# Kernel optimization log

Measured on AMD Instinct MI355X. Metric: run time of the kernel, lower is better.

## Reference

```python
import jax, jax.numpy as jnp
import numpy as np

N_NODES = 100000
N_EDGES = 400000
N_REL = 3
N_LAYERS = 2
D = 128          # input feature dim == hidden_dim so weights stack cleanly
N_CLASSES = 2


def setup_inputs() -> dict:
    key = jax.random.key(0)
    ks = jax.random.split(key, 7)
    x = jax.random.normal(ks[0], (N_NODES, D), dtype=jnp.float32)
    edge_index = jax.random.randint(ks[1], (N_REL, 2, N_EDGES), 0, N_NODES, dtype=jnp.int32)
    # SAGEConv params per (layer, relation): neighbor weight, root weight, bias
    Wn = jax.random.normal(ks[2], (N_LAYERS, N_REL, D, D), dtype=jnp.float32) * (1.0 / np.sqrt(D))
    Wr = jax.random.normal(ks[3], (N_LAYERS, N_REL, D, D), dtype=jnp.float32) * (1.0 / np.sqrt(D))
    b = jax.random.normal(ks[4], (N_LAYERS, N_REL, D), dtype=jnp.float32) * 0.02
    Wc = jax.random.normal(ks[5], (D, N_CLASSES), dtype=jnp.float32) * (1.0 / np.sqrt(D))
    bc = jax.random.normal(ks[6], (N_CLASSES,), dtype=jnp.float32) * 0.02
    return {"x": x, "edge_index": edge_index, "Wn": Wn, "Wr": Wr, "b": b, "Wc": Wc, "bc": bc}


def _mean_agg(h, ei, n_nodes):
    # gather source features, scatter-mean into destination nodes
    src, dst = ei[0], ei[1]
    s = jax.ops.segment_sum(h[src], dst, num_segments=n_nodes)          # [N, D]
    cnt = jax.ops.segment_sum(jnp.ones((ei.shape[1],), h.dtype), dst, num_segments=n_nodes)
    return s / jnp.maximum(cnt, 1.0)[:, None]


def reference(x, edge_index, Wn, Wr, b, Wc, bc):
    n = x.shape[0]
    h = x
    L, R = Wn.shape[0], Wn.shape[1]
    for l in range(L):
        out = jnp.zeros((n, Wn.shape[-1]), h.dtype)
        for r in range(R):
            # SAGEConv: lin_l(mean neighbors) + lin_r(root) + bias; HeteroConv sums relations
            agg = _mean_agg(h, edge_index[r], n)
            out = out + agg @ Wn[l, r] + h @ Wr[l, r] + b[l, r]
        h = jax.nn.relu(out) if l < L - 1 else out  # dropout is eval-mode identity
    return h @ Wc + bc
```

## Files before the change

kernel.cpp:

```cpp
#include <hip/hip_runtime.h>

#define NN 100000
#define NE 400000
#define NR 3
#define DD 128
#define NROWS (NR * NN)
#define NEDGES (NR * NE)
#define SCAN_BLOCKS ((NROWS + 1023) / 1024)

typedef float f32x4 __attribute__((ext_vector_type(4)));
typedef __bf16 bf16x8 __attribute__((ext_vector_type(8)));

__device__ __forceinline__ unsigned short f2bf(float f) {
    unsigned int u = __float_as_uint(f);
    u += 0x7fff + ((u >> 16) & 1);
    return (unsigned short)(u >> 16);
}
__device__ __forceinline__ float bflo(unsigned int u) { return __uint_as_float(u << 16); }
__device__ __forceinline__ float bfhi(unsigned int u) { return __uint_as_float(u & 0xffff0000u); }

__device__ __forceinline__ void gload16(const void* g, void* l) {
    __builtin_amdgcn_global_load_lds(
        (const __attribute__((address_space(1))) void*)g,
        (__attribute__((address_space(3))) void*)l, 16, 0, 0);
}

#define NB_CVT 6250
#define NB_WT 512
#define NB_ZERO 586
__global__ __launch_bounds__(256) void prep_all(const float* __restrict__ x,
                                                const float* __restrict__ Wn,
                                                const float* __restrict__ Wr,
                                                const float* __restrict__ b,
                                                unsigned short* __restrict__ xb,
                                                unsigned short* __restrict__ Wt2,
                                                float* __restrict__ bias,
                                                unsigned int* __restrict__ zbase) {
    int bid = blockIdx.x;
    int tid = threadIdx.x;
    if (bid < NB_CVT) {
        int i = bid * 256 + tid;
        const float4* xf = reinterpret_cast<const float4*>(x + (size_t)i * 8);
        float4 a = xf[0], bv = xf[1];
        uint4 o;
        o.x = (unsigned)f2bf(a.x) | ((unsigned)f2bf(a.y) << 16);
        o.y = (unsigned)f2bf(a.z) | ((unsigned)f2bf(a.w) << 16);
        o.z = (unsigned)f2bf(bv.x) | ((unsigned)f2bf(bv.y) << 16);
        o.w = (unsigned)f2bf(bv.z) | ((unsigned)f2bf(bv.w) << 16);
        reinterpret_cast<uint4*>(xb)[i] = o;
    } else if (bid < NB_CVT + NB_WT) {
        int t = (bid - NB_CVT) * 256 + tid;
        int l = t >> 16;
        int rem = t & 65535;
        int n512 = rem >> 7;
        int kk = rem & 127;
        int rk = n512 >> 7, n = n512 & 127;
        float v;
        if (rk < 3) {
            v = Wn[(((size_t)l * 3 + rk) * 128 + kk) * 128 + n];
        } else {
            const float* WrL = Wr + (size_t)l * 3 * 128 * 128;
            v = WrL[kk * 128 + n] + WrL[128 * 128 + kk * 128 + n] + WrL[2 * 128 * 128 + kk * 128 + n];
        }
        Wt2[t] = f2bf(v);
    } else if (bid == NB_CVT + NB_WT) {
        int l = tid >> 7, n = tid & 127;
        bias[tid] = b[l * 384 + n] + b[l * 384 + 128 + n] + b[l * 384 + 256 + n];
    } else {
        int i = (bid - NB_CVT - NB_WT - 1) * 256 + tid;
        if (i < 150000) reinterpret_cast<uint4*>(zbase)[i] = make_uint4(0, 0, 0, 0);
    }
}

__global__ __launch_bounds__(256) void csr_count(const int* __restrict__ ei,
                                                 int* __restrict__ cnt) {
    int t = blockIdx.x * 256 + threadIdx.x;
    if (t >= NEDGES) return;
    int r = t / NE;
    int e = t - r * NE;
    int dst = ei[(r * 2 + 1) * NE + e];
    atomicAdd(&cnt[dst * 3 + r], 1);
}

__global__ __launch_bounds__(256) void scan1(const int* __restrict__ cnt,
                                             int* __restrict__ row_start,
                                             int* __restrict__ bsum) {
    __shared__ int sh[256];
    int b0 = blockIdx.x * 1024;
    int t = threadIdx.x;
    int v[4];
    int s = 0;
    #pragma unroll
    for (int j = 0; j < 4; ++j) {
        int idx = b0 + t * 4 + j;
        v[j] = (idx < NROWS) ? cnt[idx] : 0;
        s += v[j];
    }
    sh[t] = s;
    __syncthreads();
    for (int off = 1; off < 256; off <<= 1) {
        int val = (t >= off) ? sh[t - off] : 0;
        __syncthreads();
        sh[t] += val;
        __syncthreads();
    }
    int excl = (t == 0) ? 0 : sh[t - 1];
    if (t == 255) bsum[blockIdx.x] = sh[255];
    #pragma unroll
    for (int j = 0; j < 4; ++j) {
        int idx = b0 + t * 4 + j;
        if (idx < NROWS) { row_start[idx] = excl; excl += v[j]; }
    }
}

__global__ __launch_bounds__(512) void scan2(int* __restrict__ bsum, int nb) {
    __shared__ int sh[512];
    int t = threadIdx.x;
    sh[t] = (t < nb) ? bsum[t] : 0;
    __syncthreads();
    for (int off = 1; off < 512; off <<= 1) {
        int val = (t >= off) ? sh[t - off] : 0;
        __syncthreads();
        sh[t] += val;
        __syncthreads();
    }
    int excl = (t == 0) ? 0 : sh[t - 1];
    if (t < nb) bsum[t] = excl;
}

__global__ __launch_bounds__(256) void csr_fill(const int* __restrict__ ei,
                                                const int* __restrict__ row_start,
                                                const int* __restrict__ bsum,
                                                const int* __restrict__ cnt,
                                                int* __restrict__ cursor,
                                                int2* __restrict__ bucket2) {
    int t = blockIdx.x * 256 + threadIdx.x;
    if (t >= NEDGES) return;
    int r = t / NE;
    int e = t - r * NE;
    int src = ei[(r * 2 + 0) * NE + e];
    int dst = ei[(r * 2 + 1) * NE + e];
    int i = dst * 3 + r;
    int pos = row_start[i] + bsum[i >> 10] + atomicAdd(&cursor[i], 1);
    float sc = 1.0f / (float)cnt[i];
    bucket2[pos] = make_int2((src << 10) | (r << 8), __float_as_int(sc));
}

__global__ __launch_bounds__(256) void gemm_y(
    const unsigned short* __restrict__ Ab,
    const unsigned short* __restrict__ WtL,
    unsigned short* __restrict__ Yb)
{
    __shared__ __align__(16) unsigned short As[2 * 128 * 32];
    __shared__ __align__(16) unsigned short Bs[2 * 128 * 32];
    const int t = threadIdx.x;
    const int w = t >> 6, lane = t & 63;
    const int bid = blockIdx.x;
    const int p = bid & 3;
    const int m0 = (bid >> 2) * 128;
    const unsigned short* WtP = WtL + p * 128 * 128;
    const int wr = w >> 1, wcol = w & 1;
    const int fr = lane & 15;
    const int fq = lane >> 4;
    const int gsw = (((lane & 3) ^ ((lane >> 2) & 3) ^ ((lane >> 4) & 3))) * 8;
    const int rsw = (fq ^ ((fr ^ (fr >> 2)) & 3)) * 8;
    f32x4 acc[4][4] = {};

    auto stage = [&](int s, int buf) {
        const int k0 = s * 32;
        #pragma unroll
        for (int i = 0; i < 2; ++i) {
            int row = i * 64 + w * 16 + (lane >> 2);
            int grow = m0 + row;
            if (grow > NN - 1) grow = NN - 1;
            const unsigned short* gA = Ab + (size_t)grow * DD + k0 + gsw;
            gload16(gA, (char*)As + buf * 8192 + i * 4096 + w * 1024);
            const unsigned short* gB = WtP + (size_t)row * 128 + k0 + gsw;
            gload16(gB, (char*)Bs + buf * 8192 + i * 4096 + w * 1024);
        }
    };

    stage(0, 0);
    #pragma unroll
    for (int s = 0; s < 4; ++s) {
        const int cur = s & 1;
        __syncthreads();
        if (s + 1 < 4) stage(s + 1, cur ^ 1);
        const unsigned short* As_c = As + cur * 4096;
        const unsigned short* Bs_c = Bs + cur * 4096;
        bf16x8 af[4], bfr[4];
        #pragma unroll
        for (int m = 0; m < 4; ++m)
            af[m] = *reinterpret_cast<const bf16x8*>(As_c + (wr * 64 + m * 16 + fr) * 32 + rsw);
        #pragma unroll
        for (int n = 0; n < 4; ++n)
            bfr[n] = *reinterpret_cast<const bf16x8*>(Bs_c + (wcol * 64 + n * 16 + fr) * 32 + rsw);
        #pragma unroll
        for (int m = 0; m < 4; ++m)
            #pragma unroll
            for (int n = 0; n < 4; ++n)
                acc[m][n] = __builtin_amdgcn_mfma_f32_16x16x32_bf16(af[m], bfr[n], acc[m][n], 0, 0, 0);
    }

    #pragma unroll
    for (int n = 0; n < 4; ++n) {
        int col = p * 128 + wcol * 64 + n * 16 + fr;
        #pragma unroll
        for (int m = 0; m < 4; ++m) {
            int rbase = m0 + wr * 64 + m * 16 + fq * 4;
            #pragma unroll
            for (int j = 0; j < 4; ++j) {
                int row = rbase + j;
                if (row < NN) Yb[(size_t)row * 512 + col] = f2bf(acc[m][n][j]);
            }
        }
    }
}

template <int FINAL>
__global__ __launch_bounds__(256) void gather_fused(
    const unsigned short* __restrict__ Yb,
    const int2* __restrict__ bucket2,
    const int* __restrict__ row_start,
    const int* __restrict__ bsum,
    const int* __restrict__ cnt,
    const float* __restrict__ biasL,
    const float* __restrict__ Wc,
    const float* __restrict__ bc,
    unsigned short* __restrict__ hout,
    float* __restrict__ out)
{
    int wid = (blockIdx.x * 256 + threadIdx.x) >> 6;
    int lane = threadIdx.x & 63;
    if (wid >= NN) return;
    const int g = lane >> 4;
    const int q = lane & 15;
    const unsigned int qoff = q * 16u;
    const char* Yc = (const char*)Yb;
    const int r3 = wid * 3;
    const int base = row_start[r3] + bsum[r3 >> 10];
    const int degT = cnt[r3] + cnt[r3 + 1] + cnt[r3 + 2];

    float acc[8] = {};
    int e = 0;
    for (; e + 8 <= degT; e += 8) {
        int2 ma = bucket2[base + e + g];
        int2 mb = bucket2[base + e + 4 + g];
        uint4 va = *(const uint4*)(Yc + (unsigned)ma.x + qoff);
        uint4 vb = *(const uint4*)(Yc + (unsigned)mb.x + qoff);
        float sa = __int_as_float(ma.y);
        float sb = __int_as_float(mb.y);
        acc[0] = fmaf(bflo(va.x), sa, acc[0]); acc[1] = fmaf(bfhi(va.x), sa, acc[1]);
        acc[2] = fmaf(bflo(va.y), sa, acc[2]); acc[3] = fmaf(bfhi(va.y), sa, acc[3]);
        acc[4] = fmaf(bflo(va.z), sa, acc[4]); acc[5] = fmaf(bfhi(va.z), sa, acc[5]);
        acc[6] = fmaf(bflo(va.w), sa, acc[6]); acc[7] = fmaf(bfhi(va.w), sa, acc[7]);
        acc[0] = fmaf(bflo(vb.x), sb, acc[0]); acc[1] = fmaf(bfhi(vb.x), sb, acc[1]);
        acc[2] = fmaf(bflo(vb.y), sb, acc[2]); acc[3] = fmaf(bfhi(vb.y), sb, acc[3]);
        acc[4] = fmaf(bflo(vb.z), sb, acc[4]); acc[5] = fmaf(bfhi(vb.z), sb, acc[5]);
        acc[6] = fmaf(bflo(vb.w), sb, acc[6]); acc[7] = fmaf(bfhi(vb.w), sb, acc[7]);
    }
    for (; e < degT; e += 4) {
        if (e + g < degT) {
            int2 m = bucket2[base + e + g];
            uint4 v = *(const uint4*)(Yc + (unsigned)m.x + qoff);
            float s = __int_as_float(m.y);
            acc[0] = fmaf(bflo(v.x), s, acc[0]); acc[1] = fmaf(bfhi(v.x), s, acc[1]);
            acc[2] = fmaf(bflo(v.y), s, acc[2]); acc[3] = fmaf(bfhi(v.y), s, acc[3]);
            acc[4] = fmaf(bflo(v.z), s, acc[4]); acc[5] = fmaf(bfhi(v.z), s, acc[5]);
            acc[6] = fmaf(bflo(v.w), s, acc[6]); acc[7] = fmaf(bfhi(v.w), s, acc[7]);
        }
    }
    #pragma unroll
    for (int j = 0; j < 8; ++j) {
        acc[j] += __shfl_xor(acc[j], 16);
        acc[j] += __shfl_xor(acc[j], 32);
    }
    uint4 rv = *(const uint4*)(Yc + (size_t)wid * 1024u + 768u + qoff);
    acc[0] += bflo(rv.x); acc[1] += bfhi(rv.x);
    acc[2] += bflo(rv.y); acc[3] += bfhi(rv.y);
    acc[4] += bflo(rv.z); acc[5] += bfhi(rv.z);
    acc[6] += bflo(rv.w); acc[7] += bfhi(rv.w);
    float4 b0 = *(const float4*)(biasL + q * 8);
    float4 b1 = *(const float4*)(biasL + q * 8 + 4);
    acc[0] += b0.x; acc[1] += b0.y; acc[2] += b0.z; acc[3] += b0.w;
    acc[4] += b1.x; acc[5] += b1.y; acc[6] += b1.z; acc[7] += b1.w;

    if (!FINAL) {
        if (g == 0) {
            uint4 o;
            o.x = (unsigned)f2bf(fmaxf(acc[0], 0.f)) | ((unsigned)f2bf(fmaxf(acc[1], 0.f)) << 16);
            o.y = (unsigned)f2bf(fmaxf(acc[2], 0.f)) | ((unsigned)f2bf(fmaxf(acc[3], 0.f)) << 16);
            o.z = (unsigned)f2bf(fmaxf(acc[4], 0.f)) | ((unsigned)f2bf(fmaxf(acc[5], 0.f)) << 16);
            o.w = (unsigned)f2bf(fmaxf(acc[6], 0.f)) | ((unsigned)f2bf(fmaxf(acc[7], 0.f)) << 16);
            *reinterpret_cast<uint4*>(hout + (size_t)wid * DD + q * 8) = o;
        }
    } else {
        float4 w0 = *(const float4*)(Wc + q * 16);
        float4 w1 = *(const float4*)(Wc + q * 16 + 4);
        float4 w2 = *(const float4*)(Wc + q * 16 + 8);
        float4 w3 = *(const float4*)(Wc + q * 16 + 12);
        float p0 = acc[0] * w0.x + acc[1] * w0.z + acc[2] * w1.x + acc[3] * w1.z +
                   acc[4] * w2.x + acc[5] * w2.z + acc[6] * w3.x + acc[7] * w3.z;
        float p1 = acc[0] * w0.y + acc[1] * w0.w + acc[2] * w1.y + acc[3] * w1.w +
                   acc[4] * w2.y + acc[5] * w2.w + acc[6] * w3.y + acc[7] * w3.w;
        #pragma unroll
        for (int off = 1; off < 16; off <<= 1) {
            p0 += __shfl_xor(p0, off);
            p1 += __shfl_xor(p1, off);
        }
        if (lane == 0) {
            out[(size_t)wid * 2 + 0] = p0 + bc[0];
            out[(size_t)wid * 2 + 1] = p1 + bc[1];
        }
    }
}

extern "C" void kernel_launch(void* const* d_in, const int* in_sizes, int n_in,
                              void* d_out, int out_size, void* d_ws, size_t ws_size,
                              hipStream_t stream) {
    const float* x  = (const float*)d_in[0];
    const int*   ei = (const int*)d_in[1];
    const float* Wn = (const float*)d_in[2];
    const float* Wr = (const float*)d_in[3];
    const float* b  = (const float*)d_in[4];
    const float* Wc = (const float*)d_in[5];
    const float* bc = (const float*)d_in[6];
    float* out = (float*)d_out;

    char* p = (char*)d_ws;
    unsigned short* Yb  = (unsigned short*)p;  p += (size_t)NN * 512 * 2;
    unsigned short* xb  = (unsigned short*)p;  p += (size_t)NN * DD * 2;
    unsigned short* h1b = (unsigned short*)p;  p += (size_t)NN * DD * 2;
    unsigned short* Wt2 = (unsigned short*)p;  p += (size_t)2 * 4 * 128 * 128 * 2;
    float* bias         = (float*)p;           p += 2 * 128 * 4;
    int2* bucket2       = (int2*)p;            p += (size_t)NEDGES * 8;
    int* row_start      = (int*)p;             p += (size_t)NROWS * 4;
    int* bsum           = (int*)p;             p += 512 * 4;
    int* cnt            = (int*)p;             p += (size_t)NROWS * 4;
    int* cursor         = (int*)p;             p += (size_t)NROWS * 4;

    prep_all<<<NB_CVT + NB_WT + 1 + NB_ZERO, 256, 0, stream>>>(
        x, Wn, Wr, b, xb, Wt2, bias, (unsigned int*)cnt);

    csr_count<<<(NEDGES + 255) / 256, 256, 0, stream>>>(ei, cnt);
    scan1<<<SCAN_BLOCKS, 256, 0, stream>>>(cnt, row_start, bsum);
    scan2<<<1, 512, 0, stream>>>(bsum, SCAN_BLOCKS);
    csr_fill<<<(NEDGES + 255) / 256, 256, 0, stream>>>(ei, row_start, bsum, cnt, cursor, bucket2);

    const int gemmBlocks = ((NN + 127) / 128) * 4;
    const int gatherBlocks = NN * 64 / 256;

    gemm_y<<<gemmBlocks, 256, 0, stream>>>(xb, Wt2, Yb);
    gather_fused<0><<<gatherBlocks, 256, 0, stream>>>(Yb, bucket2, row_start, bsum, cnt,
                                                      bias, nullptr, nullptr, h1b, nullptr);

    gemm_y<<<gemmBlocks, 256, 0, stream>>>(h1b, Wt2 + (size_t)4 * 128 * 128, Yb);
    gather_fused<1><<<gatherBlocks, 256, 0, stream>>>(Yb, bucket2, row_start, bsum, cnt,
                                                      bias + 128, Wc, bc, nullptr, out);
}
```

Before: 441.4 us.

## Fuse edge counting into prep kernel and co-schedule CSR fill with layer-1 GEMM

Edge-degree counting is merged into the prep kernel, so input conversion and the atomic counting run in one launch. Zeroing of the count and cursor arrays moves to hipMemsetAsync calls. The CSR fill and the first-layer GEMM are merged into one kernel whose blocks alternate roles, so the atomic-heavy scatter overlaps the MFMA GEMM and two launches disappear. The cost is that fill blocks reserve the GEMM's shared memory, which can lower occupancy, and two memset calls are added.

```diff
diff --git a/kernel.cpp b/kernel.cpp
--- a/kernel.cpp
+++ b/kernel.cpp
@@ -27,15 +27,16 @@
 
 #define NB_CVT 6250
 #define NB_WT 512
-#define NB_ZERO 586
-__global__ __launch_bounds__(256) void prep_all(const float* __restrict__ x,
-                                                const float* __restrict__ Wn,
-                                                const float* __restrict__ Wr,
-                                                const float* __restrict__ b,
-                                                unsigned short* __restrict__ xb,
-                                                unsigned short* __restrict__ Wt2,
-                                                float* __restrict__ bias,
-                                                unsigned int* __restrict__ zbase) {
+#define NB_CNT 4688
+__global__ __launch_bounds__(256) void prep_count(const float* __restrict__ x,
+                                                  const float* __restrict__ Wn,
+                                                  const float* __restrict__ Wr,
+                                                  const float* __restrict__ b,
+                                                  const int* __restrict__ ei,
+                                                  unsigned short* __restrict__ xb,
+                                                  unsigned short* __restrict__ Wt2,
+                                                  float* __restrict__ bias,
+                                                  int* __restrict__ cnt) {
     int bid = blockIdx.x;
     int tid = threadIdx.x;
     if (bid < NB_CVT) {
@@ -67,19 +68,14 @@
         int l = tid >> 7, n = tid & 127;
         bias[tid] = b[l * 384 + n] + b[l * 384 + 128 + n] + b[l * 384 + 256 + n];
     } else {
-        int i = (bid - NB_CVT - NB_WT - 1) * 256 + tid;
-        if (i < 150000) reinterpret_cast<uint4*>(zbase)[i] = make_uint4(0, 0, 0, 0);
-    }
-}
-
-__global__ __launch_bounds__(256) void csr_count(const int* __restrict__ ei,
-                                                 int* __restrict__ cnt) {
-    int t = blockIdx.x * 256 + threadIdx.x;
-    if (t >= NEDGES) return;
-    int r = t / NE;
-    int e = t - r * NE;
-    int dst = ei[(r * 2 + 1) * NE + e];
-    atomicAdd(&cnt[dst * 3 + r], 1);
+        int t = (bid - NB_CVT - NB_WT - 1) * 256 + tid;
+        if (t < NEDGES) {
+            int r = t / NE;
+            int e = t - r * NE;
+            int dst = ei[(r * 2 + 1) * NE + e];
+            atomicAdd(&cnt[dst * 3 + r], 1);
+        }
+    }
 }
 
 __global__ __launch_bounds__(256) void scan1(const int* __restrict__ cnt,
@@ -128,36 +124,18 @@
     if (t < nb) bsum[t] = excl;
 }
 
-__global__ __launch_bounds__(256) void csr_fill(const int* __restrict__ ei,
-                                                const int* __restrict__ row_start,
-                                                const int* __restrict__ bsum,
-                                                const int* __restrict__ cnt,
-                                                int* __restrict__ cursor,
-                                                int2* __restrict__ bucket2) {
-    int t = blockIdx.x * 256 + threadIdx.x;
-    if (t >= NEDGES) return;
-    int r = t / NE;
-    int e = t - r * NE;
-    int src = ei[(r * 2 + 0) * NE + e];
-    int dst = ei[(r * 2 + 1) * NE + e];
-    int i = dst * 3 + r;
-    int pos = row_start[i] + bsum[i >> 10] + atomicAdd(&cursor[i], 1);
-    float sc = 1.0f / (float)cnt[i];
-    bucket2[pos] = make_int2((src << 10) | (r << 8), __float_as_int(sc));
-}
-
-__global__ __launch_bounds__(256) void gemm_y(
-    const unsigned short* __restrict__ Ab,
-    const unsigned short* __restrict__ WtL,
-    unsigned short* __restrict__ Yb)
-{
-    __shared__ __align__(16) unsigned short As[2 * 128 * 32];
-    __shared__ __align__(16) unsigned short Bs[2 * 128 * 32];
+#define NGEMM 3128
+#define NFILL 4688
+
+__device__ __forceinline__ void gemm_body(int id,
+                                          const unsigned short* __restrict__ Ab,
+                                          const unsigned short* __restrict__ WtL,
+                                          unsigned short* __restrict__ Yb,
+                                          unsigned short* As, unsigned short* Bs) {
     const int t = threadIdx.x;
     const int w = t >> 6, lane = t & 63;
-    const int bid = blockIdx.x;
-    const int p = bid & 3;
-    const int m0 = (bid >> 2) * 128;
+    const int p = id & 3;
+    const int m0 = (id >> 2) * 128;
     const unsigned short* WtP = WtL + p * 128 * 128;
     const int wr = w >> 1, wcol = w & 1;
     const int fr = lane & 15;
@@ -215,6 +193,51 @@
             }
         }
     }
+}
+
+__global__ __launch_bounds__(256) void fill_gemm(
+    const int* __restrict__ ei,
+    const int* __restrict__ row_start,
+    const int* __restrict__ bsum,
+    const int* __restrict__ cnt,
+    int* __restrict__ cursor,
+    int2* __restrict__ bucket2,
+    const unsigned short* __restrict__ Ab,
+    const unsigned short* __restrict__ WtL,
+    unsigned short* __restrict__ Yb)
+{
+    __shared__ __align__(16) unsigned short As[2 * 128 * 32];
+    __shared__ __align__(16) unsigned short Bs[2 * 128 * 32];
+    const int bid = blockIdx.x;
+    int role, id;
+    if (bid < 2 * NGEMM) { role = bid & 1; id = bid >> 1; }
+    else { role = 1; id = NGEMM + (bid - 2 * NGEMM); }
+
+    if (role == 0) {
+        gemm_body(id, Ab, WtL, Yb, As, Bs);
+    } else {
+        int t = id * 256 + threadIdx.x;
+        if (t < NEDGES) {
+            int r = t / NE;
+            int e = t - r * NE;
+            int src = ei[(r * 2 + 0) * NE + e];
+            int dst = ei[(r * 2 + 1) * NE + e];
+            int i = dst * 3 + r;
+            int pos = row_start[i] + bsum[i >> 10] + atomicAdd(&cursor[i], 1);
+            float sc = 1.0f / (float)cnt[i];
+            bucket2[pos] = make_int2((src << 10) | (r << 8), __float_as_int(sc));
+        }
+    }
+}
+
+__global__ __launch_bounds__(256) void gemm_y(
+    const unsigned short* __restrict__ Ab,
+    const unsigned short* __restrict__ WtL,
+    unsigned short* __restrict__ Yb)
+{
+    __shared__ __align__(16) unsigned short As[2 * 128 * 32];
+    __shared__ __align__(16) unsigned short Bs[2 * 128 * 32];
+    gemm_body(blockIdx.x, Ab, WtL, Yb, As, Bs);
 }
 
 template <int FINAL>
@@ -339,22 +362,25 @@
     int* cnt            = (int*)p;             p += (size_t)NROWS * 4;
     int* cursor         = (int*)p;             p += (size_t)NROWS * 4;
 
-    prep_all<<<NB_CVT + NB_WT + 1 + NB_ZERO, 256, 0, stream>>>(
-        x, Wn, Wr, b, xb, Wt2, bias, (unsigned int*)cnt);
-
-    csr_count<<<(NEDGES + 255) / 256, 256, 0, stream>>>(ei, cnt);
+    hipMemsetAsync(cnt, 0, NROWS * sizeof(int), stream);
+    hipMemsetAsync(cursor, 0, NROWS * sizeof(int), stream);
+
+    prep_count<<<NB_CVT + NB_WT + 1 + NB_CNT, 256, 0, stream>>>(
+        x, Wn, Wr, b, ei, xb, Wt2, bias, cnt);
+
     scan1<<<SCAN_BLOCKS, 256, 0, stream>>>(cnt, row_start, bsum);
     scan2<<<1, 512, 0, stream>>>(bsum, SCAN_BLOCKS);
-    csr_fill<<<(NEDGES + 255) / 256, 256, 0, stream>>>(ei, row_start, bsum, cnt, cursor, bucket2);
-
-    const int gemmBlocks = ((NN + 127) / 128) * 4;
+
+    fill_gemm<<<2 * NGEMM + (NFILL - NGEMM), 256, 0, stream>>>(
+        ei, row_start, bsum, cnt, cursor, bucket2, xb, Wt2, Yb);
+
     const int gatherBlocks = NN * 64 / 256;
 
-    gemm_y<<<gemmBlocks, 256, 0, stream>>>(xb, Wt2, Yb);
     gather_fused<0><<<gatherBlocks, 256, 0, stream>>>(Yb, bucket2, row_start, bsum, cnt,
                                                       bias, nullptr, nullptr, h1b, nullptr);
 
-    gemm_y<<<gemmBlocks, 256, 0, stream>>>(h1b, Wt2 + (size_t)4 * 128 * 128, Yb);
+    gemm_y<<<NGEMM, 256, 0, stream>>>(h1b, Wt2 + (size_t)4 * 128 * 128, Yb);
+
     gather_fused<1><<<gatherBlocks, 256, 0, stream>>>(Yb, bucket2, row_start, bsum, cnt,
                                                       bias + 128, Wc, bc, nullptr, out);
 }
```

After: 423.0 us. 1.04x faster.

## Fuse edge counting into prep, shrink CSR bucket to int, remap GEMM block order

Applied to the files above, without the earlier changes.

Merges the per-edge destination count into the prep kernel and zeroes the count and cursor buffers with hipMemsetAsync, which removes one launch. Each CSR bucket entry shrinks from an int2 to a single int, and the gather recomputes the per-relation 1/deg scale from the three counts. This halves the edge-list traffic in both gather passes at the cost of a small select per edge. The GEMM grid is remapped so eight consecutive blocks cover different row tiles for the same weight slice, aiming at better cache locality; surplus blocks exit early.

```diff
diff --git a/kernel.cpp b/kernel.cpp
--- a/kernel.cpp
+++ b/kernel.cpp
@@ -27,15 +27,16 @@
 
 #define NB_CVT 6250
 #define NB_WT 512
-#define NB_ZERO 586
-__global__ __launch_bounds__(256) void prep_all(const float* __restrict__ x,
-                                                const float* __restrict__ Wn,
-                                                const float* __restrict__ Wr,
-                                                const float* __restrict__ b,
-                                                unsigned short* __restrict__ xb,
-                                                unsigned short* __restrict__ Wt2,
-                                                float* __restrict__ bias,
-                                                unsigned int* __restrict__ zbase) {
+#define NB_CNT 4688
+__global__ __launch_bounds__(256) void prep_count(const float* __restrict__ x,
+                                                  const float* __restrict__ Wn,
+                                                  const float* __restrict__ Wr,
+                                                  const float* __restrict__ b,
+                                                  const int* __restrict__ ei,
+                                                  unsigned short* __restrict__ xb,
+                                                  unsigned short* __restrict__ Wt2,
+                                                  float* __restrict__ bias,
+                                                  int* __restrict__ cnt) {
     int bid = blockIdx.x;
     int tid = threadIdx.x;
     if (bid < NB_CVT) {
@@ -67,19 +68,14 @@
         int l = tid >> 7, n = tid & 127;
         bias[tid] = b[l * 384 + n] + b[l * 384 + 128 + n] + b[l * 384 + 256 + n];
     } else {
-        int i = (bid - NB_CVT - NB_WT - 1) * 256 + tid;
-        if (i < 150000) reinterpret_cast<uint4*>(zbase)[i] = make_uint4(0, 0, 0, 0);
-    }
-}
-
-__global__ __launch_bounds__(256) void csr_count(const int* __restrict__ ei,
-                                                 int* __restrict__ cnt) {
-    int t = blockIdx.x * 256 + threadIdx.x;
-    if (t >= NEDGES) return;
-    int r = t / NE;
-    int e = t - r * NE;
-    int dst = ei[(r * 2 + 1) * NE + e];
-    atomicAdd(&cnt[dst * 3 + r], 1);
+        int t = (bid - NB_CVT - NB_WT - 1) * 256 + tid;
+        if (t < NEDGES) {
+            int r = t / NE;
+            int e = t - r * NE;
+            int dst = ei[(r * 2 + 1) * NE + e];
+            atomicAdd(&cnt[dst * 3 + r], 1);
+        }
+    }
 }
 
 __global__ __launch_bounds__(256) void scan1(const int* __restrict__ cnt,
@@ -131,9 +127,8 @@
 __global__ __launch_bounds__(256) void csr_fill(const int* __restrict__ ei,
                                                 const int* __restrict__ row_start,
                                                 const int* __restrict__ bsum,
-                                                const int* __restrict__ cnt,
                                                 int* __restrict__ cursor,
-                                                int2* __restrict__ bucket2) {
+                                                int* __restrict__ bucket) {
     int t = blockIdx.x * 256 + threadIdx.x;
     if (t >= NEDGES) return;
     int r = t / NE;
@@ -142,10 +137,10 @@
     int dst = ei[(r * 2 + 1) * NE + e];
     int i = dst * 3 + r;
     int pos = row_start[i] + bsum[i >> 10] + atomicAdd(&cursor[i], 1);
-    float sc = 1.0f / (float)cnt[i];
-    bucket2[pos] = make_int2((src << 10) | (r << 8), __float_as_int(sc));
-}
-
+    bucket[pos] = (src << 10) | (r << 8);
+}
+
+#define NGEMM 3136
 __global__ __launch_bounds__(256) void gemm_y(
     const unsigned short* __restrict__ Ab,
     const unsigned short* __restrict__ WtL,
@@ -153,11 +148,15 @@
 {
     __shared__ __align__(16) unsigned short As[2 * 128 * 32];
     __shared__ __align__(16) unsigned short Bs[2 * 128 * 32];
+    const int bid = blockIdx.x;
+    const int x = bid & 7, j = bid >> 3;
+    const int p = j & 3;
+    const int mblk = (j >> 2) * 8 + x;
+    const int m0 = mblk * 128;
+    if (m0 >= NN) return;
+
     const int t = threadIdx.x;
     const int w = t >> 6, lane = t & 63;
-    const int bid = blockIdx.x;
-    const int p = bid & 3;
-    const int m0 = (bid >> 2) * 128;
     const unsigned short* WtP = WtL + p * 128 * 128;
     const int wr = w >> 1, wcol = w & 1;
     const int fr = lane & 15;
@@ -209,9 +208,9 @@
         for (int m = 0; m < 4; ++m) {
             int rbase = m0 + wr * 64 + m * 16 + fq * 4;
             #pragma unroll
-            for (int j = 0; j < 4; ++j) {
-                int row = rbase + j;
-                if (row < NN) Yb[(size_t)row * 512 + col] = f2bf(acc[m][n][j]);
+            for (int j2 = 0; j2 < 4; ++j2) {
+                int row = rbase + j2;
+                if (row < NN) Yb[(size_t)row * 512 + col] = f2bf(acc[m][n][j2]);
             }
         }
     }
@@ -220,7 +219,7 @@
 template <int FINAL>
 __global__ __launch_bounds__(256) void gather_fused(
     const unsigned short* __restrict__ Yb,
-    const int2* __restrict__ bucket2,
+    const int* __restrict__ bucket,
     const int* __restrict__ row_start,
     const int* __restrict__ bsum,
     const int* __restrict__ cnt,
@@ -239,17 +238,22 @@
     const char* Yc = (const char*)Yb;
     const int r3 = wid * 3;
     const int base = row_start[r3] + bsum[r3 >> 10];
-    const int degT = cnt[r3] + cnt[r3 + 1] + cnt[r3 + 2];
+    const int c0 = cnt[r3], c1 = cnt[r3 + 1], c2 = cnt[r3 + 2];
+    const int degT = c0 + c1 + c2;
+    const float i0 = 1.0f / (float)max(c0, 1);
+    const float i1 = 1.0f / (float)max(c1, 1);
+    const float i2 = 1.0f / (float)max(c2, 1);
 
     float acc[8] = {};
     int e = 0;
     for (; e + 8 <= degT; e += 8) {
-        int2 ma = bucket2[base + e + g];
-        int2 mb = bucket2[base + e + 4 + g];
-        uint4 va = *(const uint4*)(Yc + (unsigned)ma.x + qoff);
-        uint4 vb = *(const uint4*)(Yc + (unsigned)mb.x + qoff);
-        float sa = __int_as_float(ma.y);
-        float sb = __int_as_float(mb.y);
+        int ma = bucket[base + e + g];
+        int mb = bucket[base + e + 4 + g];
+        uint4 va = *(const uint4*)(Yc + (unsigned)ma + qoff);
+        uint4 vb = *(const uint4*)(Yc + (unsigned)mb + qoff);
+        int ra = (ma >> 8) & 3, rb = (mb >> 8) & 3;
+        float sa = (ra == 0) ? i0 : ((ra == 1) ? i1 : i2);
+        float sb = (rb == 0) ? i0 : ((rb == 1) ? i1 : i2);
         acc[0] = fmaf(bflo(va.x), sa, acc[0]); acc[1] = fmaf(bfhi(va.x), sa, acc[1]);
         acc[2] = fmaf(bflo(va.y), sa, acc[2]); acc[3] = fmaf(bfhi(va.y), sa, acc[3]);
         acc[4] = fmaf(bflo(va.z), sa, acc[4]); acc[5] = fmaf(bfhi(va.z), sa, acc[5]);
@@ -261,9 +265,10 @@
     }
     for (; e < degT; e += 4) {
         if (e + g < degT) {
-            int2 m = bucket2[base + e + g];
-            uint4 v = *(const uint4*)(Yc + (unsigned)m.x + qoff);
-            float s = __int_as_float(m.y);
+            int m = bucket[base + e + g];
+            uint4 v = *(const uint4*)(Yc + (unsigned)m + qoff);
+            int r = (m >> 8) & 3;
+            float s = (r == 0) ? i0 : ((r == 1) ? i1 : i2);
             acc[0] = fmaf(bflo(v.x), s, acc[0]); acc[1] = fmaf(bfhi(v.x), s, acc[1]);
             acc[2] = fmaf(bflo(v.y), s, acc[2]); acc[3] = fmaf(bfhi(v.y), s, acc[3]);
             acc[4] = fmaf(bflo(v.z), s, acc[4]); acc[5] = fmaf(bfhi(v.z), s, acc[5]);
@@ -333,28 +338,30 @@
     unsigned short* h1b = (unsigned short*)p;  p += (size_t)NN * DD * 2;
     unsigned short* Wt2 = (unsigned short*)p;  p += (size_t)2 * 4 * 128 * 128 * 2;
     float* bias         = (float*)p;           p += 2 * 128 * 4;
-    int2* bucket2       = (int2*)p;            p += (size_t)NEDGES * 8;
+    int* bucket         = (int*)p;             p += (size_t)NEDGES * 4;
     int* row_start      = (int*)p;             p += (size_t)NROWS * 4;
     int* bsum           = (int*)p;             p += 512 * 4;
     int* cnt            = (int*)p;             p += (size_t)NROWS * 4;
     int* cursor         = (int*)p;             p += (size_t)NROWS * 4;
 
-    prep_all<<<NB_CVT + NB_WT + 1 + NB_ZERO, 256, 0, stream>>>(
-        x, Wn, Wr, b, xb, Wt2, bias, (unsigned int*)cnt);
-
-    csr_count<<<(NEDGES + 255) / 256, 256, 0, stream>>>(ei, cnt);
+    hipMemsetAsync(cnt, 0, NROWS * sizeof(int), stream);
+    hipMemsetAsync(cursor, 0, NROWS * sizeof(int), stream);
+
+    prep_count<<<NB_CVT + NB_WT + 1 + NB_CNT, 256, 0, stream>>>(
+        x, Wn, Wr, b, ei, xb, Wt2, bias, cnt);
+
     scan1<<<SCAN_BLOCKS, 256, 0, stream>>>(cnt, row_start, bsum);
     scan2<<<1, 512, 0, stream>>>(bsum, SCAN_BLOCKS);
-    csr_fill<<<(NEDGES + 255) / 256, 256, 0, stream>>>(ei, row_start, bsum, cnt, cursor, bucket2);
-
-    const int gemmBlocks = ((NN + 127) / 128) * 4;
+
+    csr_fill<<<(NEDGES + 255) / 256, 256, 0, stream>>>(ei, row_start, bsum, cursor, bucket);
+
     const int gatherBlocks = NN * 64 / 256;
 
-    gemm_y<<<gemmBlocks, 256, 0, stream>>>(xb, Wt2, Yb);
-    gather_fused<0><<<gatherBlocks, 256, 0, stream>>>(Yb, bucket2, row_start, bsum, cnt,
+    gemm_y<<<NGEMM, 256, 0, stream>>>(xb, Wt2, Yb);
+    gather_fused<0><<<gatherBlocks, 256, 0, stream>>>(Yb, bucket, row_start, bsum, cnt,
                                                       bias, nullptr, nullptr, h1b, nullptr);
 
-    gemm_y<<<gemmBlocks, 256, 0, stream>>>(h1b, Wt2 + (size_t)4 * 128 * 128, Yb);
-    gather_fused<1><<<gatherBlocks, 256, 0, stream>>>(Yb, bucket2, row_start, bsum, cnt,
+    gemm_y<<<NGEMM, 256, 0, stream>>>(h1b, Wt2 + (size_t)4 * 128 * 128, Yb);
+    gather_fused<1><<<gatherBlocks, 256, 0, stream>>>(Yb, bucket, row_start, bsum, cnt,
                                                       bias + 128, Wc, bc, nullptr, out);
 }
```

New measurement: 436.5 us. No clear change (-1.1%).
